# Performance work log

Hardware: AMD Instinct MI355X
Metric: run time of the kernel (lower is better)

## Reference

```python
import jax, jax.numpy as jnp
import numpy as np
from jax.scipy.linalg import expm

D = 512      # d_model
S = 3        # num_scales
BATCH = 256
H = 8        # attention heads
HD = D // H  # head dim


def layernorm(x, g, b, eps=1e-5):
    m = jnp.mean(x, axis=-1, keepdims=True)
    v = jnp.var(x, axis=-1, keepdims=True)
    return (x - m) / jnp.sqrt(v + eps) * g + b


def setup_inputs() -> dict:
    key = jax.random.key(0)
    ks = jax.random.split(key, 16)
    sd = 1.0 / np.sqrt(D)
    inp = {
        'x': jax.random.normal(ks[0], (BATCH, D), jnp.float32),
        'h_prev': jax.random.normal(ks[1], (BATCH, D), jnp.float32),
        'lstm_h': jax.random.normal(ks[2], (S, BATCH, D), jnp.float32) * 0.1,
        'lstm_c': jax.random.normal(ks[3], (S, BATCH, D), jnp.float32) * 0.1,
        'A': jax.random.normal(ks[4], (D, D), jnp.float32) * sd,
        'Bm': jax.random.normal(ks[5], (D, D), jnp.float32) * sd,
        'dn_w1': jax.random.normal(ks[6], (D, D), jnp.float32) * sd,
        'dn_b1': jnp.zeros((D,), jnp.float32),
        'dn_g': jnp.ones((D,), jnp.float32),
        'dn_beta': jnp.zeros((D,), jnp.float32),
        'dn_w2': jax.random.normal(ks[7], (1, D), jnp.float32) * sd,
        'dn_b2': jnp.zeros((1,), jnp.float32),
        'lstm_wih': jax.random.normal(ks[8], (S, 4 * D, D), jnp.float32) * sd,
        'lstm_whh': jax.random.normal(ks[9], (S, 4 * D, D), jnp.float32) * sd,
        'lstm_bih': jnp.zeros((S, 4 * D), jnp.float32),
        'lstm_bhh': jnp.zeros((S, 4 * D), jnp.float32),
        'decays': jnp.linspace(0.5, 0.95, S, dtype=jnp.float32),
        'attn_in_w': jax.random.normal(ks[10], (3 * D, D), jnp.float32) * sd,
        'attn_in_b': jnp.zeros((3 * D,), jnp.float32),
        'attn_out_w': jax.random.normal(ks[11], (D, D), jnp.float32) * sd,
        'attn_out_b': jnp.zeros((D,), jnp.float32),
        'proj_w': jax.random.normal(ks[12], (D, (S + 2) * D), jnp.float32) * (1.0 / np.sqrt((S + 2) * D)),
        'proj_b': jnp.zeros((D,), jnp.float32),
        'proj_g': jnp.ones((D,), jnp.float32),
        'proj_beta': jnp.zeros((D,), jnp.float32),
    }
    return inp


def reference(x, h_prev, lstm_h, lstm_c, A, Bm, dn_w1, dn_b1, dn_g, dn_beta,
              dn_w2, dn_b2, lstm_wih, lstm_whh, lstm_bih, lstm_bhh, decays,
              attn_in_w, attn_in_b, attn_out_w, attn_out_b,
              proj_w, proj_b, proj_g, proj_beta):
    # ---- delta_net: Linear -> LayerNorm -> GELU(exact) -> Linear -> Softplus ----
    h1 = layernorm(x @ dn_w1.T + dn_b1, dn_g, dn_beta)
    h1 = jax.nn.gelu(h1, approximate=False)
    delta = jax.nn.softplus(h1 @ dn_w2.T + dn_b2)           # (B, 1)

    # ---- SSM update: h_t = expm(delta*A) h_prev + delta*B x ----
    A_disc = jax.vmap(expm)(delta[:, :, None] * A)          # (B, D, D)
    h_ssm = jnp.einsum('bij,bj->bi', A_disc, h_prev) + delta * jnp.einsum('ij,bj->bi', Bm, x)

    # ---- multi-scale LSTM cells (vectorized over scales) ----
    gates = (jnp.einsum('bd,skd->sbk', x, lstm_wih)
             + jnp.einsum('sbd,skd->sbk', lstm_h, lstm_whh)
             + (lstm_bih + lstm_bhh)[:, None, :])           # (S, B, 4D)
    gi, gf, gg, go = jnp.split(gates, 4, axis=-1)
    i_g = jax.nn.sigmoid(gi)
    f_g = jax.nn.sigmoid(gf)
    g_g = jnp.tanh(gg)
    o_g = jax.nn.sigmoid(go)
    c_raw = f_g * lstm_c + i_g * g_g                        # (S, B, D)
    h_new = o_g * jnp.tanh(c_raw)                           # (S, B, D)
    dec = decays[:, None, None]
    c_new = dec * lstm_c + (1.0 - dec) * c_raw              # (S, B, D)

    # ---- fusion attention: 1 query (h_ssm), S keys/values (h_new) ----
    Wq, Wk, Wv = jnp.split(attn_in_w, 3, axis=0)
    bq, bk, bv = jnp.split(attn_in_b, 3, axis=0)
    kv = jnp.transpose(h_new, (1, 0, 2))                    # (B, S, D)
    q = (h_ssm @ Wq.T + bq).reshape(-1, 1, H, HD).transpose(0, 2, 1, 3)   # (B,H,1,HD)
    k = (kv @ Wk.T + bk).reshape(-1, S, H, HD).transpose(0, 2, 1, 3)      # (B,H,S,HD)
    v = (kv @ Wv.T + bv).reshape(-1, S, H, HD).transpose(0, 2, 1, 3)
    scores = jnp.einsum('bhqe,bhke->bhqk', q, k) / np.sqrt(HD)
    attn = jax.nn.softmax(scores, axis=-1)
    ctx = jnp.einsum('bhqk,bhke->bhqe', attn, v)            # (B,H,1,HD)
    ctx = ctx.transpose(0, 2, 1, 3).reshape(-1, D)          # (B, D)
    fused = ctx @ attn_out_w.T + attn_out_b                 # (B, D)

    # ---- output projection over concat [h_ssm, fused, h_1..h_S] ----
    combined = jnp.concatenate([h_ssm, fused] + [h_new[i] for i in range(S)], axis=-1)
    output = layernorm(combined @ proj_w.T + proj_b, proj_g, proj_beta)
    return (output, h_ssm, h_new, c_new)
```

## Files before the change

kernel.cpp:

```cpp
#include <hip/hip_runtime.h>
#include <math.h>

#define DIM 512
#define NB 256
#define KMAX 16

using bf16x8 = __attribute__((ext_vector_type(8))) short;
using f32x4  = __attribute__((ext_vector_type(4))) float;
using float4v = __attribute__((ext_vector_type(4))) float;
using ushort4v = __attribute__((ext_vector_type(4))) unsigned short;

__device__ __forceinline__ unsigned short f2b(float f) {
    union { float f; unsigned int u; } v; v.f = f;
    unsigned int r = v.u + 0x7fffu + ((v.u >> 16) & 1u);
    return (unsigned short)(r >> 16);
}
__device__ __forceinline__ float b2f(unsigned short u) {
    union { unsigned int u; float f; } v; v.u = ((unsigned int)u) << 16;
    return v.f;
}
__device__ __forceinline__ ushort4v f2b4(float4v v) {
    ushort4v o;
    o.x = f2b(v.x); o.y = f2b(v.y); o.z = f2b(v.z); o.w = f2b(v.w);
    return o;
}

struct GemmDesc {
    const unsigned short* X;
    const unsigned short* W;
    const float* bias;
    float* Cf;
    unsigned short* Cb;
    unsigned short* Ct;
    int M, N, K, ldX, ldC, tr_row0;
};
struct GemmArgs { GemmDesc d[4]; };

__global__ __launch_bounds__(256) void gemm_mfma(GemmArgs args)
{
    GemmDesc de = args.d[blockIdx.y];
    int tn = de.N >> 6;
    int tiles = (de.M >> 6) * tn;
    int t = blockIdx.x;
    if (t >= tiles) return;
    int m0 = (t / tn) << 6;
    int n0 = (t % tn) << 6;

    __shared__ unsigned short lsA[2][4096];
    __shared__ unsigned short lsB[2][4096];

    int tid = threadIdx.x;
    int w = tid >> 6;
    int l = tid & 63;
    int nkt = de.K >> 6;

    int srow = w * 16 + (l >> 2);
    int schk = l & 3;
    const unsigned short* gA = de.X + (size_t)(m0 + srow) * de.ldX + schk * 8;
    const unsigned short* gB = de.W + (size_t)(n0 + srow) * de.K  + schk * 8;
    unsigned short* lA = &lsA[0][(w * 64 + l) * 8];
    unsigned short* lB = &lsB[0][(w * 64 + l) * 8];

#define STAGE(bufi, kt)                                                          \
    do {                                                                         \
        __builtin_amdgcn_global_load_lds(                                        \
            (const __attribute__((address_space(1))) unsigned int*)(gA + (size_t)(kt) * 64), \
            (__attribute__((address_space(3))) unsigned int*)(lA + (bufi) * 4096), 16, 0, 0); \
        __builtin_amdgcn_global_load_lds(                                        \
            (const __attribute__((address_space(1))) unsigned int*)(gA + (size_t)(kt) * 64 + 32), \
            (__attribute__((address_space(3))) unsigned int*)(lA + (bufi) * 4096 + 2048), 16, 0, 0); \
        __builtin_amdgcn_global_load_lds(                                        \
            (const __attribute__((address_space(1))) unsigned int*)(gB + (size_t)(kt) * 64), \
            (__attribute__((address_space(3))) unsigned int*)(lB + (bufi) * 4096), 16, 0, 0); \
        __builtin_amdgcn_global_load_lds(                                        \
            (const __attribute__((address_space(1))) unsigned int*)(gB + (size_t)(kt) * 64 + 32), \
            (__attribute__((address_space(3))) unsigned int*)(lB + (bufi) * 4096 + 2048), 16, 0, 0); \
    } while (0)

    int mbase = (w >> 1) * 32;
    int nbase = (w & 1) * 32;

    f32x4 acc[2][2];
    #pragma unroll
    for (int i = 0; i < 2; ++i)
        #pragma unroll
        for (int j = 0; j < 2; ++j)
            acc[i][j] = (f32x4){0.f, 0.f, 0.f, 0.f};

    int kg = l >> 4;
    int fr = l & 15;
    int aslot = (mbase * 4 + fr * 4 + kg) * 8;
    int bslot = (nbase * 4 + fr * 4 + kg) * 8;

    STAGE(0, 0);

    for (int kt = 0; kt < nkt; ++kt) {
        __syncthreads();
        if (kt + 1 < nkt) STAGE((kt + 1) & 1, kt + 1);

        const unsigned short* bufA = &lsA[kt & 1][0];
        const unsigned short* bufB = &lsB[kt & 1][0];
        #pragma unroll
        for (int h = 0; h < 2; ++h) {
            bf16x8 a0 = *(const bf16x8*)(bufA + h * 2048 + aslot);
            bf16x8 a1 = *(const bf16x8*)(bufA + h * 2048 + aslot + 512);
            bf16x8 b0 = *(const bf16x8*)(bufB + h * 2048 + bslot);
            bf16x8 b1 = *(const bf16x8*)(bufB + h * 2048 + bslot + 512);
            acc[0][0] = __builtin_amdgcn_mfma_f32_16x16x32_bf16(a0, b0, acc[0][0], 0, 0, 0);
            acc[0][1] = __builtin_amdgcn_mfma_f32_16x16x32_bf16(a0, b1, acc[0][1], 0, 0, 0);
            acc[1][0] = __builtin_amdgcn_mfma_f32_16x16x32_bf16(a1, b0, acc[1][0], 0, 0, 0);
            acc[1][1] = __builtin_amdgcn_mfma_f32_16x16x32_bf16(a1, b1, acc[1][1], 0, 0, 0);
        }
    }

    #pragma unroll
    for (int mi = 0; mi < 2; ++mi) {
        #pragma unroll
        for (int ni = 0; ni < 2; ++ni) {
            int col = n0 + nbase + ni * 16 + fr;
            float bv = de.bias ? de.bias[col] : 0.f;
            #pragma unroll
            for (int r = 0; r < 4; ++r) {
                int row = m0 + mbase + mi * 16 + (l >> 4) * 4 + r;
                float v = acc[mi][ni][r] + bv;
                if (de.Cf) de.Cf[(size_t)row * de.ldC + col] = v;
                else       de.Cb[(size_t)row * de.ldC + col] = f2b(v);
                if (de.Ct && row >= de.tr_row0)
                    de.Ct[(size_t)col * 512 + (row - de.tr_row0)] = f2b(v);
            }
        }
    }
#undef STAGE
}

#define NSEG 13
struct PrepArgs {
    const float* sA[NSEG]; const float* sB[NSEG]; unsigned short* dst[NSEG];
    int n4[NSEG], dRL4[NSEG], sRLA4[NSEG], sRLB4[NSEG], half4[NSEG], offA[NSEG];
    const float* A; unsigned short* ATb;
    const float* aout_w; unsigned short* aout_wT;
    const float* proj_w; const float* proj_b; const float* aout_b; float* bprime;
};
__global__ __launch_bounds__(256) void prep_kernel(PrepArgs a)
{
    __shared__ float tile[32][33];
    int bid = blockIdx.x, tid = threadIdx.x;
    if (bid < 2048) {
        const int gstride = 2048 * 256;
        int g0 = bid * 256 + tid;
        for (int seg = 0; seg < NSEG; ++seg) {
            int n4 = a.n4[seg];
            const float* sA = a.sA[seg];
            const float* sB = a.sB[seg];
            unsigned short* d = a.dst[seg];
            int dRL4 = a.dRL4[seg], sRLA4 = a.sRLA4[seg], sRLB4 = a.sRLB4[seg];
            int half4 = a.half4[seg], offA = a.offA[seg];
            for (int i = g0; i < n4; i += gstride) {
                int r = i / dRL4, c = i - r * dRL4;
                const float* src = (c < half4)
                    ? sA + ((size_t)r * sRLA4 + offA + c) * 4
                    : sB + ((size_t)r * sRLB4 + (c - half4)) * 4;
                float4v v = *(const float4v*)src;
                *(ushort4v*)(d + (size_t)i * 4) = f2b4(v);
            }
        }
    } else if (bid < 2560) {
        int t = bid - 2048;
        const float* src = (t < 256) ? a.A : a.aout_w;
        unsigned short* dst = (t < 256) ? a.ATb : a.aout_wT;
        int tt = t & 255;
        int bx = tt & 15, by = tt >> 4;
        int tx = tid & 31, ty = tid >> 5;
        #pragma unroll
        for (int i = 0; i < 32; i += 8)
            tile[ty + i][tx] = src[(size_t)(by * 32 + ty + i) * 512 + bx * 32 + tx];
        __syncthreads();
        #pragma unroll
        for (int i = 0; i < 32; i += 8)
            dst[(size_t)(bx * 32 + ty + i) * 512 + by * 32 + tx] = f2b(tile[tx][ty + i]);
    } else {
        int i = (bid - 2560) * 4 + (tid >> 6);
        int lane = tid & 63;
        float acc = 0.f;
        #pragma unroll
        for (int n = 0; n < 512; n += 64)
            acc += a.proj_w[(size_t)i * 2560 + 512 + n + lane] * a.aout_b[n + lane];
        #pragma unroll
        for (int off = 32; off > 0; off >>= 1) acc += __shfl_down(acc, off);
        if (lane == 0) a.bprime[i] = a.proj_b[i] + acc;
    }
}

__device__ __forceinline__ void block_reduce2(float& s, float& q, float* sb1, float* sb2)
{
    int tid = threadIdx.x;
    #pragma unroll
    for (int off = 32; off > 0; off >>= 1) {
        s += __shfl_down(s, off);
        q += __shfl_down(q, off);
    }
    if ((tid & 63) == 0) { sb1[tid >> 6] = s; sb2[tid >> 6] = q; }
    __syncthreads();
    s = sb1[0] + sb1[1] + sb1[2] + sb1[3];
    q = sb2[0] + sb2[1] + sb2[2] + sb2[3];
    __syncthreads();
}

__global__ __launch_bounds__(256) void ln_gelu_delta(
    const float* __restrict__ pre, const float* __restrict__ g,
    const float* __restrict__ beta, const float* __restrict__ w2,
    const float* __restrict__ b2, float* __restrict__ delta,
    float* __restrict__ coeff)
{
    __shared__ float sb1[4], sb2[4];
    int b = blockIdx.x, tid = threadIdx.x;
    int i0 = tid, i1 = tid + 256;
    float x0 = pre[(size_t)b * DIM + i0];
    float x1 = pre[(size_t)b * DIM + i1];
    float s = x0 + x1, q = x0 * x0 + x1 * x1;
    block_reduce2(s, q, sb1, sb2);
    float mean = s * (1.f / DIM);
    float var  = q * (1.f / DIM) - mean * mean;
    float inv  = rsqrtf(var + 1e-5f);
    float y0 = (x0 - mean) * inv * g[i0] + beta[i0];
    float y1 = (x1 - mean) * inv * g[i1] + beta[i1];
    float h0 = 0.5f * y0 * (1.f + erff(y0 * 0.70710678118654752f));
    float h1 = 0.5f * y1 * (1.f + erff(y1 * 0.70710678118654752f));
    float p = h0 * w2[i0] + h1 * w2[i1];
    float dummy = 0.f;
    block_reduce2(p, dummy, sb1, sb2);
    if (tid == 0) {
        float z = p + b2[0];
        float d = (z > 20.f) ? z : log1pf(expf(z));
        delta[b] = d;
        float c = 1.f;
        coeff[b] = 1.f;
        for (int k = 1; k <= KMAX; ++k) { c *= d / (float)k; coeff[k * 256 + b] = c; }
    }
}

__global__ void pointwise_fused(
    const float* __restrict__ Tm, const float* __restrict__ coeff,
    const float* __restrict__ h_prev, const float* __restrict__ delta,
    const float* __restrict__ Bx, float* __restrict__ hssm,
    unsigned short* __restrict__ combb,
    const float* __restrict__ gates, const float* __restrict__ bih,
    const float* __restrict__ bhh, const float* __restrict__ cin,
    const float* __restrict__ decays,
    float* __restrict__ hout, float* __restrict__ cout)
{
    int idx4 = blockIdx.x * 256 + threadIdx.x;
    int base = idx4 * 4;
    if (base < 131072) {
        int b = base >> 9, i = base & 511;
        const float* Tr = Tm + (size_t)b * (KMAX * DIM) + i;
        float4v a = *(const float4v*)(h_prev + base);
        #pragma unroll
        for (int k = 1; k <= KMAX; ++k) {
            float c = coeff[k * 256 + b];
            float4v t = *(const float4v*)(Tr + (size_t)(k - 1) * DIM);
            a.x += c * t.x; a.y += c * t.y; a.z += c * t.z; a.w += c * t.w;
        }
        float dl = delta[b];
        float4v bx = *(const float4v*)(Bx + base);
        a.x += dl * bx.x; a.y += dl * bx.y; a.z += dl * bx.z; a.w += dl * bx.w;
        *(float4v*)(hssm + base) = a;
        *(ushort4v*)(combb + (size_t)b * 2560 + i) = f2b4(a);
    } else {
        int i2 = base - 131072;
        int s = i2 / (NB * DIM);
        int r = i2 - s * (NB * DIM);
        int b = r >> 9, d = r & 511;
        const float* gr = gates + (size_t)s * 524288 + (size_t)b * 2048 + d;
        const float* bi = bih + s * 2048 + d;
        const float* bh = bhh + s * 2048 + d;
        float4v gi = *(const float4v*)(gr);
        float4v gf = *(const float4v*)(gr + 512);
        float4v gg = *(const float4v*)(gr + 1024);
        float4v go = *(const float4v*)(gr + 1536);
        float4v bi0 = *(const float4v*)(bi),       bh0 = *(const float4v*)(bh);
        float4v bi1 = *(const float4v*)(bi + 512), bh1 = *(const float4v*)(bh + 512);
        float4v bi2 = *(const float4v*)(bi + 1024),bh2 = *(const float4v*)(bh + 1024);
        float4v bi3 = *(const float4v*)(bi + 1536),bh3 = *(const float4v*)(bh + 1536);
        float4v c = *(const float4v*)(cin + i2);
        float dec = decays[s];
        float4v hn, cn;
        #pragma unroll
        for (int j = 0; j < 4; ++j) {
            float vgi = ((const float*)&gi)[j] + ((const float*)&bi0)[j] + ((const float*)&bh0)[j];
            float vgf = ((const float*)&gf)[j] + ((const float*)&bi1)[j] + ((const float*)&bh1)[j];
            float vgg = ((const float*)&gg)[j] + ((const float*)&bi2)[j] + ((const float*)&bh2)[j];
            float vgo = ((const float*)&go)[j] + ((const float*)&bi3)[j] + ((const float*)&bh3)[j];
            float ig = 1.f / (1.f + expf(-vgi));
            float fg = 1.f / (1.f + expf(-vgf));
            float g_ = tanhf(vgg);
            float og = 1.f / (1.f + expf(-vgo));
            float cc = ((const float*)&c)[j];
            float craw = fg * cc + ig * g_;
            ((float*)&hn)[j] = og * tanhf(craw);
            ((float*)&cn)[j] = dec * cc + (1.f - dec) * craw;
        }
        *(float4v*)(hout + i2) = hn;
        *(float4v*)(cout + i2) = cn;
        *(ushort4v*)(combb + (size_t)b * 2560 + 1024 + s * 512 + d) = f2b4(hn);
    }
}

__global__ __launch_bounds__(128) void attn_kernel(
    const unsigned short* __restrict__ qb, const unsigned short* __restrict__ kvb,
    unsigned short* __restrict__ combb)
{
    int b = blockIdx.x, t = threadIdx.x;
    int h = t >> 4, sub = (t & 15) * 4;
    int col = h * 64 + sub;
    ushort4v q4 = *(const ushort4v*)(qb + (size_t)b * 512 + col);
    float qf[4] = { b2f(q4.x), b2f(q4.y), b2f(q4.z), b2f(q4.w) };
    float p[3];
    ushort4v k4[3], v4[3];
    #pragma unroll
    for (int s = 0; s < 3; ++s) {
        k4[s] = *(const ushort4v*)(kvb + (size_t)s * 262144 + (size_t)b * 1024 + col);
        v4[s] = *(const ushort4v*)(kvb + (size_t)s * 262144 + (size_t)b * 1024 + 512 + col);
        p[s] = qf[0] * b2f(k4[s].x) + qf[1] * b2f(k4[s].y)
             + qf[2] * b2f(k4[s].z) + qf[3] * b2f(k4[s].w);
    }
    #pragma unroll
    for (int off = 1; off < 16; off <<= 1) {
        p[0] += __shfl_xor(p[0], off);
        p[1] += __shfl_xor(p[1], off);
        p[2] += __shfl_xor(p[2], off);
    }
    const float scale = 0.125f;
    float p0 = p[0] * scale, p1 = p[1] * scale, p2 = p[2] * scale;
    float m = fmaxf(p0, fmaxf(p1, p2));
    float w0 = expf(p0 - m), w1 = expf(p1 - m), w2 = expf(p2 - m);
    float invs = 1.f / (w0 + w1 + w2);
    float4v ctx;
    ((float*)&ctx)[0] = (w0 * b2f(v4[0].x) + w1 * b2f(v4[1].x) + w2 * b2f(v4[2].x)) * invs;
    ((float*)&ctx)[1] = (w0 * b2f(v4[0].y) + w1 * b2f(v4[1].y) + w2 * b2f(v4[2].y)) * invs;
    ((float*)&ctx)[2] = (w0 * b2f(v4[0].z) + w1 * b2f(v4[1].z) + w2 * b2f(v4[2].z)) * invs;
    ((float*)&ctx)[3] = (w0 * b2f(v4[0].w) + w1 * b2f(v4[1].w) + w2 * b2f(v4[2].w)) * invs;
    *(ushort4v*)(combb + (size_t)b * 2560 + 512 + col) = f2b4(ctx);
}

__global__ __launch_bounds__(256) void layernorm_k(
    const float* __restrict__ in, const float* __restrict__ g,
    const float* __restrict__ beta, float* __restrict__ outp)
{
    __shared__ float sb1[4], sb2[4];
    int b = blockIdx.x, tid = threadIdx.x;
    int i0 = tid, i1 = tid + 256;
    float x0 = in[(size_t)b * DIM + i0];
    float x1 = in[(size_t)b * DIM + i1];
    float s = x0 + x1, q = x0 * x0 + x1 * x1;
    block_reduce2(s, q, sb1, sb2);
    float mean = s * (1.f / DIM);
    float var  = q * (1.f / DIM) - mean * mean;
    float inv  = rsqrtf(var + 1e-5f);
    outp[(size_t)b * DIM + i0] = (x0 - mean) * inv * g[i0] + beta[i0];
    outp[(size_t)b * DIM + i1] = (x1 - mean) * inv * g[i1] + beta[i1];
}

extern "C" void kernel_launch(void* const* d_in, const int* in_sizes, int n_in,
                              void* d_out, int out_size, void* d_ws, size_t ws_size,
                              hipStream_t stream)
{
    const float* x        = (const float*)d_in[0];
    const float* h_prev   = (const float*)d_in[1];
    const float* lstm_h   = (const float*)d_in[2];
    const float* lstm_c   = (const float*)d_in[3];
    const float* A        = (const float*)d_in[4];
    const float* Bm       = (const float*)d_in[5];
    const float* dn_w1    = (const float*)d_in[6];
    const float* dn_b1    = (const float*)d_in[7];
    const float* dn_g     = (const float*)d_in[8];
    const float* dn_beta  = (const float*)d_in[9];
    const float* dn_w2    = (const float*)d_in[10];
    const float* dn_b2    = (const float*)d_in[11];
    const float* wih      = (const float*)d_in[12];
    const float* whh      = (const float*)d_in[13];
    const float* bih      = (const float*)d_in[14];
    const float* bhh      = (const float*)d_in[15];
    const float* decays   = (const float*)d_in[16];
    const float* ain_w    = (const float*)d_in[17];
    const float* ain_b    = (const float*)d_in[18];
    const float* aout_w   = (const float*)d_in[19];
    const float* aout_b   = (const float*)d_in[20];
    const float* proj_w   = (const float*)d_in[21];
    const float* proj_b   = (const float*)d_in[22];
    const float* proj_g   = (const float*)d_in[23];
    const float* proj_bt  = (const float*)d_in[24];

    float* out  = (float*)d_out;
    float* hssm = out + 131072;
    float* hnew = out + 262144;
    float* cnew = out + 655360;

    unsigned short* us = (unsigned short*)d_ws;
    unsigned short* hpb     = us;
    unsigned short* ATb     = us + 131072;
    unsigned short* dn_w1b  = us + 393216;
    unsigned short* Bmb     = us + 655360;
    unsigned short* ain_wb  = us + 917504;
    unsigned short* proj_wb = us + 1703936;
    unsigned short* P2b     = us + 3014656;
    unsigned short* aout_wT = us + 3276800;
    unsigned short* Pw      = us + 3538944;
    unsigned short* Qa      = us + 7733248;
    unsigned short* Qb      = us + 7995392;
    unsigned short* Wcat    = us + 8257536;
    unsigned short* Xcat    = us + 14548992;
    unsigned short* combb   = us + 15335424;
    unsigned short* qb      = us + 15990784;
    unsigned short* kvb     = us + 16121856;
    float* fbase  = (float*)(us + 16908288);
    float* pre1   = fbase;
    float* delta  = fbase + 131072;
    float* coeff  = fbase + 131328;
    float* Bx     = fbase + 135680;
    float* bprime = fbase + 266752;
    float* Tm     = fbase + 267264;
    float* gates  = fbase + 2364416;
    float* projout = pre1;

    PrepArgs pa;
    int sidx = 0;
    auto LIN = [&](const float* s, unsigned short* d, int n4) {
        pa.sA[sidx]=s; pa.sB[sidx]=s; pa.dst[sidx]=d; pa.n4[sidx]=n4;
        pa.dRL4[sidx]=n4; pa.sRLA4[sidx]=0; pa.sRLB4[sidx]=0;
        pa.half4[sidx]=n4; pa.offA[sidx]=0; ++sidx;
    };
    LIN(h_prev, hpb,     32768);
    LIN(A,      Pw,      65536);
    LIN(dn_w1,  dn_w1b,  65536);
    LIN(Bm,     Bmb,     65536);
    LIN(ain_w,  ain_wb,  196608);
    LIN(proj_w, proj_wb, 327680);
    pa.sA[sidx]=proj_w; pa.sB[sidx]=proj_w; pa.dst[sidx]=P2b; pa.n4[sidx]=65536;
    pa.dRL4[sidx]=128; pa.sRLA4[sidx]=640; pa.sRLB4[sidx]=640; pa.half4[sidx]=128; pa.offA[sidx]=128; ++sidx;
    for (int s = 0; s < 3; ++s) {
        pa.sA[sidx]=wih + (size_t)s*1048576; pa.sB[sidx]=whh + (size_t)s*1048576;
        pa.dst[sidx]=Wcat + (size_t)s*2097152; pa.n4[sidx]=524288;
        pa.dRL4[sidx]=256; pa.sRLA4[sidx]=128; pa.sRLB4[sidx]=128; pa.half4[sidx]=128; pa.offA[sidx]=0; ++sidx;
    }
    for (int s = 0; s < 3; ++s) {
        pa.sA[sidx]=x; pa.sB[sidx]=lstm_h + (size_t)s*131072;
        pa.dst[sidx]=Xcat + (size_t)s*262144; pa.n4[sidx]=65536;
        pa.dRL4[sidx]=256; pa.sRLA4[sidx]=128; pa.sRLB4[sidx]=128; pa.half4[sidx]=128; pa.offA[sidx]=0; ++sidx;
    }
    pa.A = A; pa.ATb = ATb; pa.aout_w = aout_w; pa.aout_wT = aout_wT;
    pa.proj_w = proj_w; pa.proj_b = proj_b; pa.aout_b = aout_b; pa.bprime = bprime;
    prep_kernel<<<2688, 256, 0, stream>>>(pa);

    GemmArgs ga;
    ga.d[0] = { Xcat, dn_w1b, dn_b1, pre1, nullptr, nullptr, 256, 512, 512, 1024, 512, 0 };
    ga.d[1] = { Xcat, Bmb,    nullptr, Bx,  nullptr, nullptr, 256, 512, 512, 1024, 512, 0 };
    ga.d[2] = { P2b,  aout_wT, nullptr, nullptr, proj_wb + 512, nullptr, 512, 512, 512, 512, 2560, 0 };
    ga.d[3] = { Pw, ATb, nullptr, nullptr, Pw + 1*262144, Qa, 512, 512, 512, 512, 512, 0 };
    gemm_mfma<<<dim3(64, 4), 256, 0, stream>>>(ga);
    ln_gelu_delta<<<256, 256, 0, stream>>>(pre1, dn_g, dn_beta, dn_w2, dn_b2, delta, coeff);

    ga.d[0] = { Pw, Qa, nullptr, nullptr, Pw + 2*262144, Qb, 1024, 512, 512, 512, 512, 512 };
    gemm_mfma<<<dim3(128, 1), 256, 0, stream>>>(ga);
    ga.d[0] = { Pw, Qb, nullptr, nullptr, Pw + 4*262144, Qa, 2048, 512, 512, 512, 512, 1536 };
    gemm_mfma<<<dim3(256, 1), 256, 0, stream>>>(ga);
    ga.d[0] = { Pw, Qa, nullptr, nullptr, Pw + 8*262144, nullptr, 4096, 512, 512, 512, 512, 0 };
    gemm_mfma<<<dim3(512, 1), 256, 0, stream>>>(ga);

    ga.d[0] = { hpb, Pw, nullptr, Tm, nullptr, nullptr, 256, KMAX*512, 512, 512, KMAX*512, 0 };
    for (int s = 0; s < 3; ++s)
        ga.d[1 + s] = { Xcat + (size_t)s * 262144, Wcat + (size_t)s * 2097152, nullptr,
                        gates + (size_t)s * 524288, nullptr, nullptr, 256, 2048, 1024, 1024, 2048, 0 };
    gemm_mfma<<<dim3(512, 4), 256, 0, stream>>>(ga);

    pointwise_fused<<<512, 256, 0, stream>>>(Tm, coeff, h_prev, delta, Bx, hssm, combb,
                                             gates, bih, bhh, lstm_c, decays, hnew, cnew);

    ga.d[0] = { combb, ain_wb, ain_b, nullptr, qb, nullptr, 256, 512, 512, 2560, 512, 0 };
    for (int s = 0; s < 3; ++s)
        ga.d[1 + s] = { combb + 1024 + (size_t)s * 512, ain_wb + 262144, ain_b + 512,
                        nullptr, kvb + (size_t)s * 262144, nullptr, 256, 1024, 512, 2560, 1024, 0 };
    gemm_mfma<<<dim3(64, 4), 256, 0, stream>>>(ga);
    attn_kernel<<<256, 128, 0, stream>>>(qb, kvb, combb);

    ga.d[0] = { combb, proj_wb, bprime, projout, nullptr, nullptr, 256, 512, 2560, 2560, 512, 0 };
    gemm_mfma<<<dim3(32, 1), 256, 0, stream>>>(ga);
    layernorm_k<<<256, 256, 0, stream>>>(projout, proj_g, proj_bt, out);
}
```

Measured before the change: 234.6 us.

## Fold LN-delta into GEMM launch, split output projection, rebalance Tm GEMM

Moves the LayerNorm/GELU/softplus delta computation into the gemm_mfma kernel as an extra grid row, so it runs alongside the second matrix-power GEMM instead of as its own launch. Reorders the combined buffer so that the output projection over h_ssm and the LSTM states can run in the same launch as the QKV GEMM. Only the attention-dependent part (ctx times the precomputed fused out-projection matrix) runs after attention, and it accumulates into the projection output. Also splits the Tm GEMM into two halves so the first half overlaps the LSTM gate GEMMs. The cost is an extra GEMM launch, read-modify-write accumulation, and an extra weight buffer.

Result: no change. 237.2 us (+1.1%).

```diff
diff --git a/kernel.cpp b/kernel.cpp
--- a/kernel.cpp
+++ b/kernel.cpp
@@ -23,6 +23,21 @@
     ushort4v o;
     o.x = f2b(v.x); o.y = f2b(v.y); o.z = f2b(v.z); o.w = f2b(v.w);
     return o;
+}
+
+__device__ __forceinline__ void block_reduce2(float& s, float& q, float* sb1, float* sb2)
+{
+    int tid = threadIdx.x;
+    #pragma unroll
+    for (int off = 32; off > 0; off >>= 1) {
+        s += __shfl_down(s, off);
+        q += __shfl_down(q, off);
+    }
+    if ((tid & 63) == 0) { sb1[tid >> 6] = s; sb2[tid >> 6] = q; }
+    __syncthreads();
+    s = sb1[0] + sb1[1] + sb1[2] + sb1[3];
+    q = sb2[0] + sb2[1] + sb2[2] + sb2[3];
+    __syncthreads();
 }
 
 struct GemmDesc {
@@ -32,12 +47,49 @@
     float* Cf;
     unsigned short* Cb;
     unsigned short* Ct;
-    int M, N, K, ldX, ldC, tr_row0;
+    int M, N, K, ldX, ldW, ldC, tr_row0, acc;
 };
-struct GemmArgs { GemmDesc d[4]; };
-
-__global__ __launch_bounds__(256) void gemm_mfma(GemmArgs args)
-{
+struct GemmArgs { GemmDesc d[5]; };
+struct LnParams {
+    const float* pre; const float* g; const float* beta;
+    const float* w2; const float* b2; float* delta; float* coeff;
+    int lnd_y;
+};
+
+__global__ __launch_bounds__(256) void gemm_mfma(GemmArgs args, LnParams lp)
+{
+    __shared__ unsigned short lsA[2][4096];
+    __shared__ unsigned short lsB[2][4096];
+    __shared__ float sb1[4], sb2[4];
+
+    if ((int)blockIdx.y == lp.lnd_y) {
+        int b = blockIdx.x, tid = threadIdx.x;
+        int i0 = tid, i1 = tid + 256;
+        float x0 = lp.pre[(size_t)b * DIM + i0];
+        float x1 = lp.pre[(size_t)b * DIM + i1];
+        float s = x0 + x1, q = x0 * x0 + x1 * x1;
+        block_reduce2(s, q, sb1, sb2);
+        float mean = s * (1.f / DIM);
+        float var  = q * (1.f / DIM) - mean * mean;
+        float inv  = rsqrtf(var + 1e-5f);
+        float y0 = (x0 - mean) * inv * lp.g[i0] + lp.beta[i0];
+        float y1 = (x1 - mean) * inv * lp.g[i1] + lp.beta[i1];
+        float h0 = 0.5f * y0 * (1.f + erff(y0 * 0.70710678118654752f));
+        float h1 = 0.5f * y1 * (1.f + erff(y1 * 0.70710678118654752f));
+        float p = h0 * lp.w2[i0] + h1 * lp.w2[i1];
+        float dummy = 0.f;
+        block_reduce2(p, dummy, sb1, sb2);
+        if (tid == 0) {
+            float z = p + lp.b2[0];
+            float d = (z > 20.f) ? z : log1pf(expf(z));
+            lp.delta[b] = d;
+            float c = 1.f;
+            lp.coeff[b] = 1.f;
+            for (int k = 1; k <= KMAX; ++k) { c *= d / (float)k; lp.coeff[k * 256 + b] = c; }
+        }
+        return;
+    }
+
     GemmDesc de = args.d[blockIdx.y];
     int tn = de.N >> 6;
     int tiles = (de.M >> 6) * tn;
@@ -46,9 +98,6 @@
     int m0 = (t / tn) << 6;
     int n0 = (t % tn) << 6;
 
-    __shared__ unsigned short lsA[2][4096];
-    __shared__ unsigned short lsB[2][4096];
-
     int tid = threadIdx.x;
     int w = tid >> 6;
     int l = tid & 63;
@@ -57,7 +106,7 @@
     int srow = w * 16 + (l >> 2);
     int schk = l & 3;
     const unsigned short* gA = de.X + (size_t)(m0 + srow) * de.ldX + schk * 8;
-    const unsigned short* gB = de.W + (size_t)(n0 + srow) * de.K  + schk * 8;
+    const unsigned short* gB = de.W + (size_t)(n0 + srow) * de.ldW + schk * 8;
     unsigned short* lA = &lsA[0][(w * 64 + l) * 8];
     unsigned short* lB = &lsB[0][(w * 64 + l) * 8];
 
@@ -123,8 +172,12 @@
             for (int r = 0; r < 4; ++r) {
                 int row = m0 + mbase + mi * 16 + (l >> 4) * 4 + r;
                 float v = acc[mi][ni][r] + bv;
-                if (de.Cf) de.Cf[(size_t)row * de.ldC + col] = v;
-                else       de.Cb[(size_t)row * de.ldC + col] = f2b(v);
+                if (de.Cf) {
+                    if (de.acc) de.Cf[(size_t)row * de.ldC + col] += v;
+                    else        de.Cf[(size_t)row * de.ldC + col] = v;
+                } else {
+                    de.Cb[(size_t)row * de.ldC + col] = f2b(v);
+                }
                 if (de.Ct && row >= de.tr_row0)
                     de.Ct[(size_t)col * 512 + (row - de.tr_row0)] = f2b(v);
             }
@@ -188,54 +241,6 @@
         #pragma unroll
         for (int off = 32; off > 0; off >>= 1) acc += __shfl_down(acc, off);
         if (lane == 0) a.bprime[i] = a.proj_b[i] + acc;
-    }
-}
-
-__device__ __forceinline__ void block_reduce2(float& s, float& q, float* sb1, float* sb2)
-{
-    int tid = threadIdx.x;
-    #pragma unroll
-    for (int off = 32; off > 0; off >>= 1) {
-        s += __shfl_down(s, off);
-        q += __shfl_down(q, off);
-    }
-    if ((tid & 63) == 0) { sb1[tid >> 6] = s; sb2[tid >> 6] = q; }
-    __syncthreads();
-    s = sb1[0] + sb1[1] + sb1[2] + sb1[3];
-    q = sb2[0] + sb2[1] + sb2[2] + sb2[3];
-    __syncthreads();
-}
-
-__global__ __launch_bounds__(256) void ln_gelu_delta(
-    const float* __restrict__ pre, const float* __restrict__ g,
-    const float* __restrict__ beta, const float* __restrict__ w2,
-    const float* __restrict__ b2, float* __restrict__ delta,
-    float* __restrict__ coeff)
-{
-    __shared__ float sb1[4], sb2[4];
-    int b = blockIdx.x, tid = threadIdx.x;
-    int i0 = tid, i1 = tid + 256;
-    float x0 = pre[(size_t)b * DIM + i0];
-    float x1 = pre[(size_t)b * DIM + i1];
-    float s = x0 + x1, q = x0 * x0 + x1 * x1;
-    block_reduce2(s, q, sb1, sb2);
-    float mean = s * (1.f / DIM);
-    float var  = q * (1.f / DIM) - mean * mean;
-    float inv  = rsqrtf(var + 1e-5f);
-    float y0 = (x0 - mean) * inv * g[i0] + beta[i0];
-    float y1 = (x1 - mean) * inv * g[i1] + beta[i1];
-    float h0 = 0.5f * y0 * (1.f + erff(y0 * 0.70710678118654752f));
-    float h1 = 0.5f * y1 * (1.f + erff(y1 * 0.70710678118654752f));
-    float p = h0 * w2[i0] + h1 * w2[i1];
-    float dummy = 0.f;
-    block_reduce2(p, dummy, sb1, sb2);
-    if (tid == 0) {
-        float z = p + b2[0];
-        float d = (z > 20.f) ? z : log1pf(expf(z));
-        delta[b] = d;
-        float c = 1.f;
-        coeff[b] = 1.f;
-        for (int k = 1; k <= KMAX; ++k) { c *= d / (float)k; coeff[k * 256 + b] = c; }
     }
 }
 
@@ -302,7 +307,7 @@
         }
         *(float4v*)(hout + i2) = hn;
         *(float4v*)(cout + i2) = cn;
-        *(ushort4v*)(combb + (size_t)b * 2560 + 1024 + s * 512 + d) = f2b4(hn);
+        *(ushort4v*)(combb + (size_t)b * 2560 + 512 + s * 512 + d) = f2b4(hn);
     }
 }
 
@@ -340,7 +345,7 @@
     ((float*)&ctx)[1] = (w0 * b2f(v4[0].y) + w1 * b2f(v4[1].y) + w2 * b2f(v4[2].y)) * invs;
     ((float*)&ctx)[2] = (w0 * b2f(v4[0].z) + w1 * b2f(v4[1].z) + w2 * b2f(v4[2].z)) * invs;
     ((float*)&ctx)[3] = (w0 * b2f(v4[0].w) + w1 * b2f(v4[1].w) + w2 * b2f(v4[2].w)) * invs;
-    *(ushort4v*)(combb + (size_t)b * 2560 + 512 + col) = f2b4(ctx);
+    *(ushort4v*)(combb + (size_t)b * 2560 + 2048 + col) = f2b4(ctx);
 }
 
 __global__ __launch_bounds__(256) void layernorm_k(
@@ -413,7 +418,8 @@
     unsigned short* combb   = us + 15335424;
     unsigned short* qb      = us + 15990784;
     unsigned short* kvb     = us + 16121856;
-    float* fbase  = (float*)(us + 16908288);
+    unsigned short* M2b     = us + 16908288;
+    float* fbase  = (float*)(us + 17170432);
     float* pre1   = fbase;
     float* delta  = fbase + 131072;
     float* coeff  = fbase + 131328;
@@ -422,6 +428,10 @@
     float* Tm     = fbase + 267264;
     float* gates  = fbase + 2364416;
     float* projout = pre1;
+
+    LnParams lpOff; lpOff.pre = nullptr; lpOff.g = nullptr; lpOff.beta = nullptr;
+    lpOff.w2 = nullptr; lpOff.b2 = nullptr; lpOff.delta = nullptr; lpOff.coeff = nullptr;
+    lpOff.lnd_y = -1;
 
     PrepArgs pa;
     int sidx = 0;
@@ -435,7 +445,8 @@
     LIN(dn_w1,  dn_w1b,  65536);
     LIN(Bm,     Bmb,     65536);
     LIN(ain_w,  ain_wb,  196608);
-    LIN(proj_w, proj_wb, 327680);
+    pa.sA[sidx]=proj_w; pa.sB[sidx]=proj_w + 1024; pa.dst[sidx]=proj_wb; pa.n4[sidx]=262144;
+    pa.dRL4[sidx]=512; pa.sRLA4[sidx]=640; pa.sRLB4[sidx]=640; pa.half4[sidx]=128; pa.offA[sidx]=0; ++sidx;
     pa.sA[sidx]=proj_w; pa.sB[sidx]=proj_w; pa.dst[sidx]=P2b; pa.n4[sidx]=65536;
     pa.dRL4[sidx]=128; pa.sRLA4[sidx]=640; pa.sRLB4[sidx]=640; pa.half4[sidx]=128; pa.offA[sidx]=128; ++sidx;
     for (int s = 0; s < 3; ++s) {
@@ -453,37 +464,44 @@
     prep_kernel<<<2688, 256, 0, stream>>>(pa);
 
     GemmArgs ga;
-    ga.d[0] = { Xcat, dn_w1b, dn_b1, pre1, nullptr, nullptr, 256, 512, 512, 1024, 512, 0 };
-    ga.d[1] = { Xcat, Bmb,    nullptr, Bx,  nullptr, nullptr, 256, 512, 512, 1024, 512, 0 };
-    ga.d[2] = { P2b,  aout_wT, nullptr, nullptr, proj_wb + 512, nullptr, 512, 512, 512, 512, 2560, 0 };
-    ga.d[3] = { Pw, ATb, nullptr, nullptr, Pw + 1*262144, Qa, 512, 512, 512, 512, 512, 0 };
-    gemm_mfma<<<dim3(64, 4), 256, 0, stream>>>(ga);
-    ln_gelu_delta<<<256, 256, 0, stream>>>(pre1, dn_g, dn_beta, dn_w2, dn_b2, delta, coeff);
-
-    ga.d[0] = { Pw, Qa, nullptr, nullptr, Pw + 2*262144, Qb, 1024, 512, 512, 512, 512, 512 };
-    gemm_mfma<<<dim3(128, 1), 256, 0, stream>>>(ga);
-    ga.d[0] = { Pw, Qb, nullptr, nullptr, Pw + 4*262144, Qa, 2048, 512, 512, 512, 512, 1536 };
-    gemm_mfma<<<dim3(256, 1), 256, 0, stream>>>(ga);
-    ga.d[0] = { Pw, Qa, nullptr, nullptr, Pw + 8*262144, nullptr, 4096, 512, 512, 512, 512, 0 };
-    gemm_mfma<<<dim3(512, 1), 256, 0, stream>>>(ga);
-
-    ga.d[0] = { hpb, Pw, nullptr, Tm, nullptr, nullptr, 256, KMAX*512, 512, 512, KMAX*512, 0 };
+    ga.d[0] = { Xcat, dn_w1b, dn_b1, pre1, nullptr, nullptr, 256, 512, 512, 1024, 512, 512, 0, 0 };
+    ga.d[1] = { Xcat, Bmb,    nullptr, Bx,  nullptr, nullptr, 256, 512, 512, 1024, 512, 512, 0, 0 };
+    ga.d[2] = { P2b,  aout_wT, nullptr, nullptr, M2b, nullptr, 512, 512, 512, 512, 512, 512, 0, 0 };
+    ga.d[3] = { Pw, ATb, nullptr, nullptr, Pw + 1*262144, Qa, 512, 512, 512, 512, 512, 512, 0, 0 };
+    gemm_mfma<<<dim3(64, 4), 256, 0, stream>>>(ga, lpOff);
+
+    LnParams lp1 = { pre1, dn_g, dn_beta, dn_w2, dn_b2, delta, coeff, 1 };
+    ga.d[0] = { Pw, Qa, nullptr, nullptr, Pw + 2*262144, Qb, 1024, 512, 512, 512, 512, 512, 512, 0 };
+    ga.d[1] = ga.d[0];
+    gemm_mfma<<<dim3(256, 2), 256, 0, stream>>>(ga, lp1);
+
+    ga.d[0] = { Pw, Qb, nullptr, nullptr, Pw + 4*262144, Qa, 2048, 512, 512, 512, 512, 512, 1536, 0 };
+    gemm_mfma<<<dim3(256, 1), 256, 0, stream>>>(ga, lpOff);
+
+    ga.d[0] = { Pw, Qa, nullptr, nullptr, Pw + 8*262144, nullptr, 4096, 512, 512, 512, 512, 512, 0, 0 };
+    ga.d[1] = { hpb, Pw, nullptr, Tm, nullptr, nullptr, 256, 4096, 512, 512, 512, 8192, 0, 0 };
     for (int s = 0; s < 3; ++s)
-        ga.d[1 + s] = { Xcat + (size_t)s * 262144, Wcat + (size_t)s * 2097152, nullptr,
-                        gates + (size_t)s * 524288, nullptr, nullptr, 256, 2048, 1024, 1024, 2048, 0 };
-    gemm_mfma<<<dim3(512, 4), 256, 0, stream>>>(ga);
+        ga.d[2 + s] = { Xcat + (size_t)s * 262144, Wcat + (size_t)s * 2097152, nullptr,
+                        gates + (size_t)s * 524288, nullptr, nullptr, 256, 2048, 1024, 1024, 1024, 2048, 0, 0 };
+    gemm_mfma<<<dim3(512, 5), 256, 0, stream>>>(ga, lpOff);
+
+    ga.d[0] = { hpb, Pw + 8*262144, nullptr, Tm + 4096, nullptr, nullptr, 256, 4096, 512, 512, 512, 8192, 0, 0 };
+    gemm_mfma<<<dim3(256, 1), 256, 0, stream>>>(ga, lpOff);
 
     pointwise_fused<<<512, 256, 0, stream>>>(Tm, coeff, h_prev, delta, Bx, hssm, combb,
                                              gates, bih, bhh, lstm_c, decays, hnew, cnew);
 
-    ga.d[0] = { combb, ain_wb, ain_b, nullptr, qb, nullptr, 256, 512, 512, 2560, 512, 0 };
+    ga.d[0] = { combb, ain_wb, ain_b, nullptr, qb, nullptr, 256, 512, 512, 2560, 512, 512, 0, 0 };
     for (int s = 0; s < 3; ++s)
-        ga.d[1 + s] = { combb + 1024 + (size_t)s * 512, ain_wb + 262144, ain_b + 512,
-                        nullptr, kvb + (size_t)s * 262144, nullptr, 256, 1024, 512, 2560, 1024, 0 };
-    gemm_mfma<<<dim3(64, 4), 256, 0, stream>>>(ga);
+        ga.d[1 + s] = { combb + 512 + (size_t)s * 512, ain_wb + 262144, ain_b + 512,
+                        nullptr, kvb + (size_t)s * 262144, nullptr, 256, 1024, 512, 2560, 512, 1024, 0, 0 };
+    ga.d[4] = { combb, proj_wb, bprime, projout, nullptr, nullptr, 256, 512, 2048, 2560, 2048, 512, 0, 0 };
+    gemm_mfma<<<dim3(64, 5), 256, 0, stream>>>(ga, lpOff);
+
     attn_kernel<<<256, 128, 0, stream>>>(qb, kvb, combb);
 
-    ga.d[0] = { combb, proj_wb, bprime, projout, nullptr, nullptr, 256, 512, 2560, 2560, 512, 0 };
-    gemm_mfma<<<dim3(32, 1), 256, 0, stream>>>(ga);
+    ga.d[0] = { combb + 2048, M2b, nullptr, projout, nullptr, nullptr, 256, 512, 512, 2560, 512, 512, 0, 1 };
+    gemm_mfma<<<dim3(32, 1), 256, 0, stream>>>(ga, lpOff);
+
     layernorm_k<<<256, 256, 0, stream>>>(projout, proj_g, proj_bt, out);
 }
```
